# Kernel tuning notes

Hardware: AMD Instinct MI355X
Metric: run time of the kernel (lower is better)

## Reference

```python
import jax, jax.numpy as jnp
import numpy as np

TEMPERATURE = 0.1
LISTWISE_W = 1.0
HARD_NEG_K = 32
MARGIN = 0.5
PAIRWISE_W = 0.5
NEG = jnp.float32(-1e30)  # finite stand-in for -inf (avoids inf-inf NaNs)


def _masked_segment_lse(vals, mask, idx, num_segments):
    """Stable segment-wise logsumexp over vals where mask is True."""
    v = jnp.where(mask, vals, NEG)
    m = jax.ops.segment_max(v, idx, num_segments=num_segments)  # [G]
    ex = jnp.where(mask, jnp.exp(vals - m[idx]), 0.0)
    s = jax.ops.segment_sum(ex, idx, num_segments=num_segments)
    tiny = jnp.finfo(vals.dtype).tiny
    return m + jnp.log(jnp.maximum(s, tiny))


def setup_inputs() -> dict:
    key = jax.random.key(0)
    k1, k2 = jax.random.split(key)
    G, L = 4096, 512  # graphs x edges-per-graph
    E = G * L
    logits = jax.random.normal(k1, (E,), dtype=jnp.float32)
    targets = (jax.random.uniform(k2, (E,)) < 0.1).astype(jnp.float32)
    edge_batch = jnp.repeat(jnp.arange(G, dtype=jnp.int32), L)  # sorted segment ids
    return {"logits": logits, "targets": targets, "edge_batch": edge_batch, "num_graphs": G}


def reference(logits, targets, edge_batch, num_graphs):
    G = int(num_graphs)
    E = logits.shape[0]
    L = E // G  # equal-size segments by construction

    # ---- listwise term ----
    scaled = logits / TEMPERATURE
    all_mask = jnp.ones_like(logits, dtype=bool)
    log_denom = _masked_segment_lse(scaled, all_mask, edge_batch, G)
    # (every graph has edges here, so the has_edge zeroing in torch is a no-op)
    pos_mask = targets > 0.5
    log_num = _masked_segment_lse(scaled, pos_mask, edge_batch, G)
    pos_cnt = jax.ops.segment_sum(pos_mask.astype(jnp.float32), edge_batch, num_segments=G)
    has_pos = pos_cnt > 0
    log_num_safe = jnp.where(has_pos, log_num, log_denom)
    listwise_den = jnp.maximum(jnp.sum(has_pos.astype(jnp.float32)), 1.0)
    listwise = jnp.sum(-(log_num_safe - log_denom)) / listwise_den

    # ---- pairwise hard-negative term ----
    k = HARD_NEG_K
    lg = logits.reshape(G, L)
    pos2 = (targets > 0.5).reshape(G, L)
    neg_vals = jnp.where(pos2, NEG, lg)
    hard, _ = jax.lax.top_k(neg_vals, k)  # [G, k], descending
    neg_cnt = jnp.sum(~pos2, axis=1)
    kg = jnp.minimum(neg_cnt, k)  # per-graph k = min(hard_neg_k, #neg)
    valid_n = jnp.arange(k)[None, :] < kg[:, None]  # [G, k]
    hard = jnp.where(valid_n, hard, NEG)
    # softplus(margin + z_n - z_p) over pos p x top-k negatives n: [G, L, k]
    pair = jax.nn.softplus(MARGIN + hard[:, None, :] - lg[:, :, None])
    pm = pos2[:, :, None] & valid_n[:, None, :]
    psum = jnp.sum(jnp.where(pm, pair, 0.0), axis=(1, 2))  # [G]
    Pg = jnp.sum(pos2, axis=1).astype(jnp.float32)
    kgf = kg.astype(jnp.float32)
    active = (Pg > 0) & (kgf > 0)
    contrib = jnp.where(active, psum / jnp.maximum(Pg * kgf, 1.0), 0.0)
    n_pg = jnp.sum(active.astype(jnp.float32))
    pairwise = jnp.sum(contrib) / jnp.maximum(n_pg, 1.0)

    return LISTWISE_W * listwise + PAIRWISE_W * pairwise
```

## Files before the change

### kernel.cpp

```cpp
#include <hip/hip_runtime.h>
#include <math.h>

#define L        512
#define BLK      256
#define WPB      4
#define KTOP     32
#define NEGV     (-1e30f)

#define LOG2E    1.4426950408889634f
#define LOG2E10  14.426950408889634f
#define LN2      0.6931471805599453f
#define M_L2E    0.7213475204444817f

#if __has_builtin(__builtin_amdgcn_exp2f)
#define EXP2F(x) __builtin_amdgcn_exp2f(x)
#else
#define EXP2F(x) exp2f(x)
#endif
#if __has_builtin(__builtin_amdgcn_logf)
#define LOG2F(x) __builtin_amdgcn_logf(x)
#else
#define LOG2F(x) __log2f(x)
#endif

__device__ __forceinline__ float softplus_l2(float x2) {
    return fmaxf(x2, 0.0f) + LOG2F(1.0f + EXP2F(fminf(x2, -x2)));
}

__device__ __forceinline__ unsigned lanes_below(unsigned long long m) {
    return __builtin_amdgcn_mbcnt_hi((unsigned)(m >> 32),
           __builtin_amdgcn_mbcnt_lo((unsigned)(m & 0xffffffffull), 0u));
}

__global__ __launch_bounds__(BLK) void graph_loss_kernel(
    const float* __restrict__ logits,
    const float* __restrict__ targets,
    int G,
    float* __restrict__ partials )
{
    __shared__ float pos_s[WPB][L];
    __shared__ float hard_s[WPB][KTOP];
    __shared__ float wres[WPB][4];

    const int tid  = threadIdx.x;
    const int lane = tid & 63;
    const int w    = tid >> 6;
    const int g    = blockIdx.x * WPB + w;
    const bool valid = (g < G);

    float lw = 0.0f, contrib = 0.0f, hp = 0.0f, act = 0.0f;

    if (valid) {
        const float4* lg4 = (const float4*)(logits  + (size_t)g * L);
        const float4* tg4 = (const float4*)(targets + (size_t)g * L);
        const float4 la = lg4[lane * 2], lb = lg4[lane * 2 + 1];
        const float4 ta = tg4[lane * 2], tb = tg4[lane * 2 + 1];
        float v[8]  = {la.x, la.y, la.z, la.w, lb.x, lb.y, lb.z, lb.w};
        float tv[8] = {ta.x, ta.y, ta.z, ta.w, tb.x, tb.y, tb.z, tb.w};
        bool  p[8];
        unsigned nu[8];

#pragma unroll
        for (int e = 0; e < 8; e++) {
            p[e] = tv[e] > 0.5f;
            const unsigned i = __float_as_uint(v[e]);
            const unsigned msk = (unsigned)((int)i >> 31) | 0x80000000u;
            nu[e] = p[e] ? 0u : (i ^ msk);
        }

        int pbase = 0;
#pragma unroll
        for (int e = 0; e < 8; e++) {
            const unsigned long long m = __ballot((int)p[e]);
            if (p[e]) pos_s[w][pbase + lanes_below(m)] = v[e] * LOG2E;
            pbase += __popcll(m);
        }
        const int P = pbase;

        float u[8];
        float s_mx = NEGV;
#pragma unroll
        for (int e = 0; e < 8; e++) {
            u[e] = v[e] * LOG2E10;
            s_mx = fmaxf(s_mx, u[e]);
        }
#pragma unroll
        for (int off = 32; off; off >>= 1)
            s_mx = fmaxf(s_mx, __shfl_xor(s_mx, off, 64));

        float se_all = 0.0f, se_pos = 0.0f;
#pragma unroll
        for (int e = 0; e < 8; e++) {
            const float ep = EXP2F(u[e] - s_mx);
            se_all += ep;
            se_pos += p[e] ? ep : 0.0f;
        }
#pragma unroll
        for (int off = 32; off; off >>= 1) {
            se_all += __shfl_xor(se_all, off, 64);
            se_pos += __shfl_xor(se_pos, off, 64);
        }

        if (P > 0) {
            hp = 1.0f;
            lw = LN2 * (LOG2F(se_all) - LOG2F(se_pos));
        }
        const int neg_cnt = L - P;
        const int K = neg_cnt < KTOP ? neg_cnt : KTOP;

        if (P > 0 && K > 0) {
            unsigned prefix = 0u;
            int exact = 0;
            for (int b = 31; b >= 0; --b) {
                const unsigned cand = prefix | (1u << b);
                int cnt = 0;
#pragma unroll
                for (int e = 0; e < 8; e++)
                    cnt += __popcll(__ballot(nu[e] >= cand));
                if (cnt >= K) {
                    prefix = cand;
                    if (cnt == K) { exact = 1; break; }
                }
            }
            const unsigned lo = prefix - (unsigned)exact;
            const unsigned ti = prefix ^ ((prefix & 0x80000000u) ? 0x80000000u
                                                                 : 0xFFFFFFFFu);
            const float tval = __uint_as_float(ti);
            const float tc2  = fmaf(tval, LOG2E, M_L2E);

            int hbase = 0;
#pragma unroll
            for (int e = 0; e < 8; e++) {
                const bool gt = nu[e] > lo;
                const unsigned long long m = __ballot((int)gt);
                if (gt) hard_s[w][hbase + lanes_below(m)] =
                            fmaf(v[e], LOG2E, M_L2E);
                hbase += __popcll(m);
            }
            const int c_gt = hbase;

            float psum = 0.0f;
            if (K == KTOP) {
                const float hc = (lane < c_gt) ? hard_s[w][lane & (KTOP - 1)]
                                               : tc2;
                for (int base = 0; base < P; base += 64) {
                    const float qs = pos_s[w][base + lane];
                    float a0 = 0.0f, a1 = 0.0f, a2 = 0.0f, a3 = 0.0f;
#pragma unroll
                    for (int n = 0; n < KTOP; n += 4) {
                        a0 += softplus_l2(__shfl(hc, n + 0, 64) - qs);
                        a1 += softplus_l2(__shfl(hc, n + 1, 64) - qs);
                        a2 += softplus_l2(__shfl(hc, n + 2, 64) - qs);
                        a3 += softplus_l2(__shfl(hc, n + 3, 64) - qs);
                    }
                    const float s = (a0 + a1) + (a2 + a3);
                    psum += (base + lane < P) ? s : 0.0f;
                }
            } else {
                for (int n = 0; n < c_gt; n++) {
                    const float c2 = hard_s[w][n];
                    for (int pp = lane; pp < P; pp += 64)
                        psum += softplus_l2(c2 - pos_s[w][pp]);
                }
                if (K > c_gt) {
                    float t = 0.0f;
                    for (int pp = lane; pp < P; pp += 64)
                        t += softplus_l2(tc2 - pos_s[w][pp]);
                    psum += (float)(K - c_gt) * t;
                }
            }
#pragma unroll
            for (int off = 32; off; off >>= 1)
                psum += __shfl_xor(psum, off, 64);
            contrib = LN2 * psum / fmaxf((float)P * (float)K, 1.0f);
            act = 1.0f;
        }
    }

    if (lane == 0) {
        wres[w][0] = lw;
        wres[w][1] = hp;
        wres[w][2] = contrib;
        wres[w][3] = act;
    }
    __syncthreads();
    if (tid < 4) {
        partials[blockIdx.x * 4 + tid] =
            wres[0][tid] + wres[1][tid] + wres[2][tid] + wres[3][tid];
    }
}

__global__ __launch_bounds__(256) void finalize_kernel(
    const float* __restrict__ partials, int nblocks, float* __restrict__ out)
{
    float s0 = 0, s1 = 0, s2 = 0, s3 = 0;
    for (int i = threadIdx.x; i < nblocks; i += 256) {
        const float4 p = ((const float4*)partials)[i];
        s0 += p.x; s1 += p.y; s2 += p.z; s3 += p.w;
    }
#pragma unroll
    for (int off = 32; off; off >>= 1) {
        s0 += __shfl_xor(s0, off, 64);
        s1 += __shfl_xor(s1, off, 64);
        s2 += __shfl_xor(s2, off, 64);
        s3 += __shfl_xor(s3, off, 64);
    }
    __shared__ float red[4][4];
    const int lane = threadIdx.x & 63, wid = threadIdx.x >> 6;
    if (lane == 0) { red[wid][0]=s0; red[wid][1]=s1; red[wid][2]=s2; red[wid][3]=s3; }
    __syncthreads();
    if (threadIdx.x == 0) {
        const float a0 = red[0][0]+red[1][0]+red[2][0]+red[3][0];
        const float a1 = red[0][1]+red[1][1]+red[2][1]+red[3][1];
        const float a2 = red[0][2]+red[1][2]+red[2][2]+red[3][2];
        const float a3 = red[0][3]+red[1][3]+red[2][3]+red[3][3];
        const float listwise = a0 / fmaxf(a1, 1.0f);
        const float pairwise = a2 / fmaxf(a3, 1.0f);
        out[0] = 1.0f * listwise + 0.5f * pairwise;
    }
}

extern "C" void kernel_launch(void* const* d_in, const int* in_sizes, int n_in,
                              void* d_out, int out_size, void* d_ws, size_t ws_size,
                              hipStream_t stream) {
    const float* logits  = (const float*)d_in[0];
    const float* targets = (const float*)d_in[1];
    const int E = in_sizes[0];
    const int G = E / L;
    const int nblocks = (G + WPB - 1) / WPB;

    float* partials = (float*)d_ws;
    graph_loss_kernel<<<nblocks, BLK, 0, stream>>>(logits, targets, G, partials);
    finalize_kernel<<<1, 256, 0, stream>>>(partials, nblocks, (float*)d_out);
}
```

Before: 81.18 us.

## Split listwise and pairwise work across separate waves per graph

```diff
diff --git a/kernel.cpp b/kernel.cpp
--- a/kernel.cpp
+++ b/kernel.cpp
@@ -3,7 +3,7 @@
 
 #define L        512
 #define BLK      256
-#define WPB      4
+#define GPB      2
 #define KTOP     32
 #define NEGV     (-1e30f)
 
@@ -38,17 +38,17 @@
     int G,
     float* __restrict__ partials )
 {
-    __shared__ float pos_s[WPB][L];
-    __shared__ float hard_s[WPB][KTOP];
-    __shared__ float wres[WPB][4];
+    __shared__ float pos_s[GPB][L];
+    __shared__ float hard_s[GPB][KTOP];
+    __shared__ float wres[GPB][4];
 
     const int tid  = threadIdx.x;
     const int lane = tid & 63;
     const int w    = tid >> 6;
-    const int g    = blockIdx.x * WPB + w;
+    const int role = w >> 1;
+    const int slot = w & 1;
+    const int g    = blockIdx.x * GPB + slot;
     const bool valid = (g < G);
-
-    float lw = 0.0f, contrib = 0.0f, hp = 0.0f, act = 0.0f;
 
     if (valid) {
         const float4* lg4 = (const float4*)(logits  + (size_t)g * L);
@@ -58,135 +58,141 @@
         float v[8]  = {la.x, la.y, la.z, la.w, lb.x, lb.y, lb.z, lb.w};
         float tv[8] = {ta.x, ta.y, ta.z, ta.w, tb.x, tb.y, tb.z, tb.w};
         bool  p[8];
-        unsigned nu[8];
-
-#pragma unroll
-        for (int e = 0; e < 8; e++) {
-            p[e] = tv[e] > 0.5f;
-            const unsigned i = __float_as_uint(v[e]);
-            const unsigned msk = (unsigned)((int)i >> 31) | 0x80000000u;
-            nu[e] = p[e] ? 0u : (i ^ msk);
+#pragma unroll
+        for (int e = 0; e < 8; e++) p[e] = tv[e] > 0.5f;
+
+        if (role == 0) {
+            float u[8];
+            float s_mx = NEGV;
+            int   pcnt = 0;
+#pragma unroll
+            for (int e = 0; e < 8; e++) {
+                u[e] = v[e] * LOG2E10;
+                s_mx = fmaxf(s_mx, u[e]);
+                pcnt += p[e] ? 1 : 0;
+            }
+#pragma unroll
+            for (int off = 32; off; off >>= 1)
+                s_mx = fmaxf(s_mx, __shfl_xor(s_mx, off, 64));
+
+            float se_all = 0.0f, se_pos = 0.0f;
+#pragma unroll
+            for (int e = 0; e < 8; e++) {
+                const float ep = EXP2F(u[e] - s_mx);
+                se_all += ep;
+                se_pos += p[e] ? ep : 0.0f;
+            }
+            float pc = (float)pcnt;
+#pragma unroll
+            for (int off = 32; off; off >>= 1) {
+                se_all += __shfl_xor(se_all, off, 64);
+                se_pos += __shfl_xor(se_pos, off, 64);
+                pc     += __shfl_xor(pc, off, 64);
+            }
+            float lw = 0.0f, hp = 0.0f;
+            if (pc > 0.0f) {
+                hp = 1.0f;
+                lw = LN2 * (LOG2F(se_all) - LOG2F(se_pos));
+            }
+            if (lane == 0) { wres[slot][0] = lw; wres[slot][1] = hp; }
+        } else {
+            unsigned nu[8];
+#pragma unroll
+            for (int e = 0; e < 8; e++) {
+                const unsigned i = __float_as_uint(v[e]);
+                const unsigned msk = (unsigned)((int)i >> 31) | 0x80000000u;
+                nu[e] = p[e] ? 0u : (i ^ msk);
+            }
+
+            int pbase = 0;
+#pragma unroll
+            for (int e = 0; e < 8; e++) {
+                const unsigned long long m = __ballot((int)p[e]);
+                if (p[e]) pos_s[slot][pbase + lanes_below(m)] = v[e] * LOG2E;
+                pbase += __popcll(m);
+            }
+            const int P = pbase;
+            const int neg_cnt = L - P;
+            const int K = neg_cnt < KTOP ? neg_cnt : KTOP;
+
+            float contrib = 0.0f, act = 0.0f;
+            if (P > 0 && K > 0) {
+                unsigned prefix = 0u;
+                int exact = 0;
+                for (int b = 31; b >= 0; --b) {
+                    const unsigned cand = prefix | (1u << b);
+                    int cnt = 0;
+#pragma unroll
+                    for (int e = 0; e < 8; e++)
+                        cnt += __popcll(__ballot(nu[e] >= cand));
+                    if (cnt >= K) {
+                        prefix = cand;
+                        if (cnt == K) { exact = 1; break; }
+                    }
+                }
+                const unsigned lo = prefix - (unsigned)exact;
+                const unsigned ti = prefix ^ ((prefix & 0x80000000u)
+                                              ? 0x80000000u : 0xFFFFFFFFu);
+                const float tval = __uint_as_float(ti);
+                const float tc2  = fmaf(tval, LOG2E, M_L2E);
+
+                int hbase = 0;
+#pragma unroll
+                for (int e = 0; e < 8; e++) {
+                    const bool gt = nu[e] > lo;
+                    const unsigned long long m = __ballot((int)gt);
+                    if (gt) hard_s[slot][hbase + lanes_below(m)] =
+                                fmaf(v[e], LOG2E, M_L2E);
+                    hbase += __popcll(m);
+                }
+                const int c_gt = hbase;
+
+                float psum = 0.0f;
+                if (K == KTOP) {
+                    const float hc = (lane < c_gt)
+                                   ? hard_s[slot][lane & (KTOP - 1)] : tc2;
+                    for (int base = 0; base < P; base += 64) {
+                        const float qs = pos_s[slot][base + lane];
+                        float a0 = 0.0f, a1 = 0.0f, a2 = 0.0f, a3 = 0.0f;
+#pragma unroll
+                        for (int n = 0; n < KTOP; n += 4) {
+                            a0 += softplus_l2(__shfl(hc, n + 0, 64) - qs);
+                            a1 += softplus_l2(__shfl(hc, n + 1, 64) - qs);
+                            a2 += softplus_l2(__shfl(hc, n + 2, 64) - qs);
+                            a3 += softplus_l2(__shfl(hc, n + 3, 64) - qs);
+                        }
+                        const float s = (a0 + a1) + (a2 + a3);
+                        psum += (base + lane < P) ? s : 0.0f;
+                    }
+                } else {
+                    for (int n = 0; n < c_gt; n++) {
+                        const float c2 = hard_s[slot][n];
+                        for (int pp = lane; pp < P; pp += 64)
+                            psum += softplus_l2(c2 - pos_s[slot][pp]);
+                    }
+                    if (K > c_gt) {
+                        float t = 0.0f;
+                        for (int pp = lane; pp < P; pp += 64)
+                            t += softplus_l2(tc2 - pos_s[slot][pp]);
+                        psum += (float)(K - c_gt) * t;
+                    }
+                }
+#pragma unroll
+                for (int off = 32; off; off >>= 1)
+                    psum += __shfl_xor(psum, off, 64);
+                contrib = LN2 * psum / fmaxf((float)P * (float)K, 1.0f);
+                act = 1.0f;
+            }
+            if (lane == 0) { wres[slot][2] = contrib; wres[slot][3] = act; }
         }
-
-        int pbase = 0;
-#pragma unroll
-        for (int e = 0; e < 8; e++) {
-            const unsigned long long m = __ballot((int)p[e]);
-            if (p[e]) pos_s[w][pbase + lanes_below(m)] = v[e] * LOG2E;
-            pbase += __popcll(m);
-        }
-        const int P = pbase;
-
-        float u[8];
-        float s_mx = NEGV;
-#pragma unroll
-        for (int e = 0; e < 8; e++) {
-            u[e] = v[e] * LOG2E10;
-            s_mx = fmaxf(s_mx, u[e]);
-        }
-#pragma unroll
-        for (int off = 32; off; off >>= 1)
-            s_mx = fmaxf(s_mx, __shfl_xor(s_mx, off, 64));
-
-        float se_all = 0.0f, se_pos = 0.0f;
-#pragma unroll
-        for (int e = 0; e < 8; e++) {
-            const float ep = EXP2F(u[e] - s_mx);
-            se_all += ep;
-            se_pos += p[e] ? ep : 0.0f;
-        }
-#pragma unroll
-        for (int off = 32; off; off >>= 1) {
-            se_all += __shfl_xor(se_all, off, 64);
-            se_pos += __shfl_xor(se_pos, off, 64);
-        }
-
-        if (P > 0) {
-            hp = 1.0f;
-            lw = LN2 * (LOG2F(se_all) - LOG2F(se_pos));
-        }
-        const int neg_cnt = L - P;
-        const int K = neg_cnt < KTOP ? neg_cnt : KTOP;
-
-        if (P > 0 && K > 0) {
-            unsigned prefix = 0u;
-            int exact = 0;
-            for (int b = 31; b >= 0; --b) {
-                const unsigned cand = prefix | (1u << b);
-                int cnt = 0;
-#pragma unroll
-                for (int e = 0; e < 8; e++)
-                    cnt += __popcll(__ballot(nu[e] >= cand));
-                if (cnt >= K) {
-                    prefix = cand;
-                    if (cnt == K) { exact = 1; break; }
-                }
-            }
-            const unsigned lo = prefix - (unsigned)exact;
-            const unsigned ti = prefix ^ ((prefix & 0x80000000u) ? 0x80000000u
-                                                                 : 0xFFFFFFFFu);
-            const float tval = __uint_as_float(ti);
-            const float tc2  = fmaf(tval, LOG2E, M_L2E);
-
-            int hbase = 0;
-#pragma unroll
-            for (int e = 0; e < 8; e++) {
-                const bool gt = nu[e] > lo;
-                const unsigned long long m = __ballot((int)gt);
-                if (gt) hard_s[w][hbase + lanes_below(m)] =
-                            fmaf(v[e], LOG2E, M_L2E);
-                hbase += __popcll(m);
-            }
-            const int c_gt = hbase;
-
-            float psum = 0.0f;
-            if (K == KTOP) {
-                const float hc = (lane < c_gt) ? hard_s[w][lane & (KTOP - 1)]
-                                               : tc2;
-                for (int base = 0; base < P; base += 64) {
-                    const float qs = pos_s[w][base + lane];
-                    float a0 = 0.0f, a1 = 0.0f, a2 = 0.0f, a3 = 0.0f;
-#pragma unroll
-                    for (int n = 0; n < KTOP; n += 4) {
-                        a0 += softplus_l2(__shfl(hc, n + 0, 64) - qs);
-                        a1 += softplus_l2(__shfl(hc, n + 1, 64) - qs);
-                        a2 += softplus_l2(__shfl(hc, n + 2, 64) - qs);
-                        a3 += softplus_l2(__shfl(hc, n + 3, 64) - qs);
-                    }
-                    const float s = (a0 + a1) + (a2 + a3);
-                    psum += (base + lane < P) ? s : 0.0f;
-                }
-            } else {
-                for (int n = 0; n < c_gt; n++) {
-                    const float c2 = hard_s[w][n];
-                    for (int pp = lane; pp < P; pp += 64)
-                        psum += softplus_l2(c2 - pos_s[w][pp]);
-                }
-                if (K > c_gt) {
-                    float t = 0.0f;
-                    for (int pp = lane; pp < P; pp += 64)
-                        t += softplus_l2(tc2 - pos_s[w][pp]);
-                    psum += (float)(K - c_gt) * t;
-                }
-            }
-#pragma unroll
-            for (int off = 32; off; off >>= 1)
-                psum += __shfl_xor(psum, off, 64);
-            contrib = LN2 * psum / fmaxf((float)P * (float)K, 1.0f);
-            act = 1.0f;
-        }
-    }
-
-    if (lane == 0) {
-        wres[w][0] = lw;
-        wres[w][1] = hp;
-        wres[w][2] = contrib;
-        wres[w][3] = act;
-    }
+    } else if (lane == 0) {
+        if (role == 0) { wres[slot][0] = 0.0f; wres[slot][1] = 0.0f; }
+        else           { wres[slot][2] = 0.0f; wres[slot][3] = 0.0f; }
+    }
+
     __syncthreads();
     if (tid < 4) {
-        partials[blockIdx.x * 4 + tid] =
-            wres[0][tid] + wres[1][tid] + wres[2][tid] + wres[3][tid];
+        partials[blockIdx.x * 4 + tid] = wres[0][tid] + wres[1][tid];
     }
 }
 
@@ -227,7 +233,7 @@
     const float* targets = (const float*)d_in[1];
     const int E = in_sizes[0];
     const int G = E / L;
-    const int nblocks = (G + WPB - 1) / WPB;
+    const int nblocks = (G + GPB - 1) / GPB;
 
     float* partials = (float*)d_ws;
     graph_loss_kernel<<<nblocks, BLK, 0, stream>>>(logits, targets, G, partials);
```

Measured after the change: 87.45 us. +7.7%, slower.
